# Kernel optimization log

Measured on AMD Instinct MI355X. Metric: run time of the kernel, lower is better.

## Reference

```python
import jax, jax.numpy as jnp
import numpy as np

IN_F = 4096
OUT_F = 4096
SEQ = 4          # sequence_length: values per codeword
NCODES = 65535   # codeword 65535 is reserved as escape in the original


def setup_inputs() -> dict:
    key = jax.random.key(0)
    k1, k2, k3, k4 = jax.random.split(key, 4)
    x = jax.random.normal(k1, (4, 2048, IN_F), dtype=jnp.float32)
    # compression table: codeword -> length-SEQ sequence of uint8 values
    table = jax.random.randint(k2, (NCODES, SEQ), 0, 256, dtype=jnp.int32)
    # compressed weight stream: OUT_F*IN_F/SEQ codeword indices
    codes = jax.random.randint(k3, (OUT_F * IN_F // SEQ,), 0, NCODES, dtype=jnp.int32)
    bias = jax.random.normal(k4, (OUT_F,), dtype=jnp.float32)
    return {"x": x, "table": table, "codes": codes, "bias": bias}


def reference(x, table, codes, bias):
    # decompress_weights: gather each codeword's sequence, flatten, view as (out, in)
    w = table[codes].reshape(OUT_F, IN_F).astype(jnp.float32)  # [O, I]
    # F.linear(x, w, bias) = x @ w.T + bias
    return jnp.einsum('bsi,oi->bso', x, w) + bias
```

## Files before the change

### kernel.cpp

```cpp
#include <hip/hip_runtime.h>

#define IN_F 4096
#define OUT_F 4096
#define M_DIM 8192
#define NT 32

typedef __attribute__((ext_vector_type(4))) int i32x4;
typedef unsigned short u16;

typedef const __attribute__((address_space(1))) void* gas_t;
typedef __attribute__((address_space(3))) void* las_t;

__device__ __forceinline__ void async16(const void* g, void* s) {
  __builtin_amdgcn_global_load_lds((gas_t)g, (las_t)s, 16, 0, 0);
}

__global__ void k_decompress8(const int* __restrict__ codes,
                              const int* __restrict__ table,
                              int* __restrict__ Wq) {
  int i = blockIdx.x * 256 + threadIdx.x;
  int4 c = *(const int4*)(codes + (size_t)i * 4);
  int4 t0 = *(const int4*)(table + (size_t)c.x * 4);
  int4 t1 = *(const int4*)(table + (size_t)c.y * 4);
  int4 t2 = *(const int4*)(table + (size_t)c.z * 4);
  int4 t3 = *(const int4*)(table + (size_t)c.w * 4);
  int4 o;
  o.x = (t0.x | (t0.y << 8) | (t0.z << 16) | (t0.w << 24)) ^ 0x80808080;
  o.y = (t1.x | (t1.y << 8) | (t1.z << 16) | (t1.w << 24)) ^ 0x80808080;
  o.z = (t2.x | (t2.y << 8) | (t2.z << 16) | (t2.w << 24)) ^ 0x80808080;
  o.w = (t3.x | (t3.y << 8) | (t3.z << 16) | (t3.w << 24)) ^ 0x80808080;
  *(int4*)(Wq + (size_t)i * 4) = o;
}

__global__ __launch_bounds__(256) void k_quantize(const float* __restrict__ x,
                                                  int* __restrict__ xq,
                                                  float* __restrict__ s,
                                                  float* __restrict__ rs2) {
  __shared__ float2 sred[4];
  const int row = blockIdx.x, t = threadIdx.x;
  const float4* xr = (const float4*)(x + (size_t)row * IN_F);
  float4 v[4];
  float amax = 0.f, sum = 0.f;
#pragma unroll
  for (int i = 0; i < 4; ++i) {
    v[i] = xr[t + i * 256];
    amax = fmaxf(amax, fmaxf(fmaxf(fabsf(v[i].x), fabsf(v[i].y)),
                             fmaxf(fabsf(v[i].z), fabsf(v[i].w))));
    sum += v[i].x + v[i].y + v[i].z + v[i].w;
  }
#pragma unroll
  for (int m = 1; m < 64; m <<= 1) {
    amax = fmaxf(amax, __shfl_xor(amax, m));
    sum += __shfl_xor(sum, m);
  }
  if ((t & 63) == 0) sred[t >> 6] = make_float2(amax, sum);
  __syncthreads();
  float2 r0 = sred[0], r1 = sred[1], r2 = sred[2], r3 = sred[3];
  amax = fmaxf(fmaxf(r0.x, r1.x), fmaxf(r2.x, r3.x));
  sum = r0.y + r1.y + r2.y + r3.y;
  const float inv = amax > 0.f ? 127.f / amax : 0.f;
  if (t == 0) { s[row] = amax / 127.f; rs2[row] = 128.f * sum; }
  int* xo = xq + (size_t)row * (IN_F / 4);
#pragma unroll
  for (int i = 0; i < 4; ++i) {
    int q0 = min(127, max(-127, __float2int_rn(v[i].x * inv)));
    int q1 = min(127, max(-127, __float2int_rn(v[i].y * inv)));
    int q2 = min(127, max(-127, __float2int_rn(v[i].z * inv)));
    int q3 = min(127, max(-127, __float2int_rn(v[i].w * inv)));
    xo[t + i * 256] = (q0 & 255) | ((q1 & 255) << 8) | ((q2 & 255) << 16) |
                      ((q3 & 255) << 24);
  }
}

#define BAR()    asm volatile("s_barrier" ::: "memory")
#define WAITV6() asm volatile("s_waitcnt vmcnt(6)" ::: "memory")
#define WAITV4() asm volatile("s_waitcnt vmcnt(4)" ::: "memory")
#define WAITV0() asm volatile("s_waitcnt vmcnt(0)" ::: "memory")
#define SBAR()   __builtin_amdgcn_sched_barrier(0)
#define MFMAI(va, vb, vc) __builtin_amdgcn_mfma_i32_16x16x64_i8((va), (vb), (vc), 0, 0, 0)

__global__ __launch_bounds__(512, 2) void k_gemm_i8(
    const char* __restrict__ Xq, const char* __restrict__ Wq,
    const float* __restrict__ s, const float* __restrict__ rs2,
    const float* __restrict__ bias, float* __restrict__ out) {
  extern __shared__ char sm[];
  const int tid = threadIdx.x;
  const int w = tid >> 6, ln = tid & 63;
  const int wr = w >> 2, wc = w & 3;

  const int orig = blockIdx.x;
  const int wg = (orig & 7) * 64 + (orig >> 3);
  const int bm0 = (wg >> 4) * 256;
  const int bn0 = (wg & 15) * 256;

  const int srow = ln >> 3;
  const int sg = ((ln & 7) ^ srow) * 16;
  const char* pA = Xq + (size_t)(bm0 + w * 16 + srow) * IN_F + sg;
  const char* pB = Wq + (size_t)(bn0 + w * 16 + srow) * IN_F + sg;
  const int wso = w * 2048;

  const int l15 = ln & 15;
  int ccp[2];
#pragma unroll
  for (int ks = 0; ks < 2; ++ks)
    ccp[ks] = ((ks * 4 + (ln >> 4)) ^ (ln & 7)) * 16;
  const int arow = (wr * 64 + l15) * 128;
  const int brow = 65536 + (wc * 32 + l15) * 128;

#define STA(t, h, db)                                                          \
  do {                                                                         \
    async16(pA + (size_t)(t)*128 + (size_t)(h)*128 * IN_F,                     \
            sm + (db)*32768 + (h)*16384 + wso);                                \
    async16(pA + (size_t)(t)*128 + (size_t)(h)*128 * IN_F + 8 * IN_F,          \
            sm + (db)*32768 + (h)*16384 + wso + 1024);                         \
  } while (0)
#define STB(t, h, db)                                                          \
  do {                                                                         \
    async16(pB + (size_t)(t)*128 + (size_t)(h)*128 * IN_F,                     \
            sm + 65536 + (db)*32768 + (h)*16384 + wso);                        \
    async16(pB + (size_t)(t)*128 + (size_t)(h)*128 * IN_F + 8 * IN_F,          \
            sm + 65536 + (db)*32768 + (h)*16384 + wso + 1024);                 \
  } while (0)
#define RD_A0(base)                                                            \
  do {                                                                         \
    _Pragma("unroll") for (int i = 0; i < 4; ++i)                              \
        _Pragma("unroll") for (int ks = 0; ks < 2; ++ks) a0[i][ks] =           \
        *(const i32x4*)(sm + (base) + arow + i * 2048 + ccp[ks]);              \
  } while (0)
#define RD_A1(base)                                                            \
  do {                                                                         \
    _Pragma("unroll") for (int i = 0; i < 4; ++i)                              \
        _Pragma("unroll") for (int ks = 0; ks < 2; ++ks) a1[i][ks] =           \
        *(const i32x4*)(sm + (base) + arow + i * 2048 + ccp[ks]);              \
  } while (0)
#define RD_B0(base)                                                            \
  do {                                                                         \
    _Pragma("unroll") for (int bn = 0; bn < 2; ++bn)                           \
        _Pragma("unroll") for (int ks = 0; ks < 2; ++ks) b0[bn][ks] =          \
        *(const i32x4*)(sm + (base) + brow + bn * 2048 + ccp[ks]);             \
  } while (0)
#define RD_B1(base)                                                            \
  do {                                                                         \
    _Pragma("unroll") for (int bn = 0; bn < 2; ++bn)                           \
        _Pragma("unroll") for (int ks = 0; ks < 2; ++ks) b1[bn][ks] =          \
        *(const i32x4*)(sm + (base) + brow + bn * 2048 + ccp[ks]);             \
  } while (0)

  STA(0, 0, 0); STB(0, 0, 0); STB(0, 1, 0); STA(0, 1, 0);
  STA(1, 0, 1); STB(1, 0, 1); STB(1, 1, 1);
  i32x4 acc[8][4] = {};
  i32x4 a0[4][2], a1[4][2], b0[2][2], b1[2][2];
  WAITV4();
  BAR();
  RD_A0(0);
  RD_B0(0);

  for (int t = 0; t < NT; ++t) {
    const int d = t & 1, dn = d ^ 1;
    const int d32 = d * 32768, dn32 = dn * 32768;
    RD_B1(d32 + 16384);
    if (t + 1 < NT) STA(t + 1, 1, dn);
    SBAR();
    __builtin_amdgcn_s_setprio(1);
#pragma unroll
    for (int i = 0; i < 4; ++i)
#pragma unroll
      for (int bn = 0; bn < 2; ++bn) {
        acc[i][bn] = MFMAI(a0[i][0], b0[bn][0], acc[i][bn]);
        acc[i][bn] = MFMAI(a0[i][1], b0[bn][1], acc[i][bn]);
      }
    __builtin_amdgcn_s_setprio(0);
    BAR();
    RD_A1(d32 + 16384);
    if (t + 2 < NT) STA(t + 2, 0, d);
    SBAR();
    __builtin_amdgcn_s_setprio(1);
#pragma unroll
    for (int i = 0; i < 4; ++i)
#pragma unroll
      for (int bn = 0; bn < 2; ++bn) {
        acc[i][2 + bn] = MFMAI(a0[i][0], b1[bn][0], acc[i][2 + bn]);
        acc[i][2 + bn] = MFMAI(a0[i][1], b1[bn][1], acc[i][2 + bn]);
      }
    __builtin_amdgcn_s_setprio(0);
    if (t + 1 < NT) RD_A0(dn32);
    if (t + 2 < NT) STB(t + 2, 0, d);
    SBAR();
    __builtin_amdgcn_s_setprio(1);
#pragma unroll
    for (int i = 0; i < 4; ++i)
#pragma unroll
      for (int bn = 0; bn < 2; ++bn) {
        acc[4 + i][2 + bn] = MFMAI(a1[i][0], b1[bn][0], acc[4 + i][2 + bn]);
        acc[4 + i][2 + bn] = MFMAI(a1[i][1], b1[bn][1], acc[4 + i][2 + bn]);
      }
    __builtin_amdgcn_s_setprio(0);
    if (t < NT - 2) { WAITV6(); } else { WAITV0(); }
    BAR();
    if (t + 2 < NT) STB(t + 2, 1, d);
    SBAR();
    __builtin_amdgcn_s_setprio(1);
#pragma unroll
    for (int i = 0; i < 4; ++i)
#pragma unroll
      for (int bn = 0; bn < 2; ++bn) {
        acc[4 + i][bn] = MFMAI(a1[i][0], b0[bn][0], acc[4 + i][bn]);
        acc[4 + i][bn] = MFMAI(a1[i][1], b0[bn][1], acc[4 + i][bn]);
      }
    __builtin_amdgcn_s_setprio(0);
    if (t + 1 < NT) RD_B0(dn32);
    if (t < NT - 2) { WAITV4(); } else { WAITV0(); }
    BAR();
  }

  const int r4 = (ln >> 4) * 4;
#pragma unroll
  for (int im = 0; im < 8; ++im) {
    const int mq = im >> 2, i = im & 3;
    const int rowb = bm0 + mq * 128 + wr * 64 + i * 16 + r4;
    float sv[4], rv[4];
#pragma unroll
    for (int r = 0; r < 4; ++r) { sv[r] = s[rowb + r]; rv[r] = rs2[rowb + r]; }
#pragma unroll
    for (int in = 0; in < 4; ++in) {
      const int nq = in >> 1, bn = in & 1;
      const int col = bn0 + nq * 128 + wc * 32 + bn * 16 + l15;
      const float bv = bias[col];
#pragma unroll
      for (int r = 0; r < 4; ++r)
        out[(size_t)(rowb + r) * OUT_F + col] =
            fmaf(sv[r], (float)acc[im][in][r], rv[r] + bv);
    }
  }
#undef STA
#undef STB
#undef RD_A0
#undef RD_A1
#undef RD_B0
#undef RD_B1
}

__global__ void k_naive(const float* __restrict__ x, const int* __restrict__ table,
                        const int* __restrict__ codes, const float* __restrict__ bias,
                        float* __restrict__ out) {
  __shared__ float sx[IN_F];
  const int m = blockIdx.y;
  const int n = blockIdx.x * 256 + threadIdx.x;
  for (int k = threadIdx.x; k < IN_F; k += 256) sx[k] = x[(size_t)m * IN_F + k];
  __syncthreads();
  float sacc = 0.f;
  const int* cr = codes + (size_t)n * (IN_F / 4);
  for (int k4 = 0; k4 < IN_F / 4; ++k4) {
    int code = cr[k4];
    int4 tt = *(const int4*)(table + (size_t)code * 4);
    const float* xp = sx + k4 * 4;
    sacc += xp[0] * tt.x + xp[1] * tt.y + xp[2] * tt.z + xp[3] * tt.w;
  }
  out[(size_t)m * OUT_F + n] = sacc + bias[n];
}

extern "C" void kernel_launch(void* const* d_in, const int* in_sizes, int n_in,
                              void* d_out, int out_size, void* d_ws, size_t ws_size,
                              hipStream_t stream) {
  const float* x = (const float*)d_in[0];
  const int* table = (const int*)d_in[1];
  const int* codes = (const int*)d_in[2];
  const float* bias = (const float*)d_in[3];
  float* out = (float*)d_out;

  const size_t wqb = (size_t)OUT_F * IN_F;
  const size_t xqb = (size_t)M_DIM * IN_F;
  const size_t sb = (size_t)M_DIM * 4;
  if (ws_size >= wqb + xqb + 2 * sb) {
    char* Wq = (char*)d_ws;
    char* Xq = (char*)d_ws + wqb;
    float* sS = (float*)((char*)d_ws + wqb + xqb);
    float* sR = sS + M_DIM;
    k_decompress8<<<(OUT_F * IN_F / 16) / 256, 256, 0, stream>>>(codes, table,
                                                                 (int*)Wq);
    k_quantize<<<M_DIM, 256, 0, stream>>>(x, (int*)Xq, sS, sR);
    (void)hipFuncSetAttribute((const void*)k_gemm_i8,
                              hipFuncAttributeMaxDynamicSharedMemorySize, 131072);
    k_gemm_i8<<<dim3((M_DIM / 256) * (OUT_F / 256)), dim3(512), 131072, stream>>>(
        Xq, Wq, sS, sR, bias, out);
  } else {
    dim3 grid(OUT_F / 256, M_DIM);
    k_naive<<<grid, 256, 0, stream>>>(x, table, codes, bias, out);
  }
}
```

Baseline: 183.6 us.

## Fuse decompress and quantize launches; drop one GEMM barrier per k-step

Merges the weight decompression and activation quantization kernels into one launch, with the grid split by block index, to save a kernel launch and the gap between the two. In the int8 GEMM main loop it removes one workgroup barrier per iteration and moves the first half of the B-tile store after the later barrier, adding an explicit LDS-count wait. Fewer barriers shorten the synchronization overhead of the software pipeline, at the risk of LDS read/write hazards if the reordered stores overlap buffers still being read.

```diff
diff --git a/kernel.cpp b/kernel.cpp
--- a/kernel.cpp
+++ b/kernel.cpp
@@ -6,7 +6,6 @@
 #define NT 32
 
 typedef __attribute__((ext_vector_type(4))) int i32x4;
-typedef unsigned short u16;
 
 typedef const __attribute__((address_space(1))) void* gas_t;
 typedef __attribute__((address_space(3))) void* las_t;
@@ -15,29 +14,28 @@
   __builtin_amdgcn_global_load_lds((gas_t)g, (las_t)s, 16, 0, 0);
 }
 
-__global__ void k_decompress8(const int* __restrict__ codes,
-                              const int* __restrict__ table,
-                              int* __restrict__ Wq) {
-  int i = blockIdx.x * 256 + threadIdx.x;
-  int4 c = *(const int4*)(codes + (size_t)i * 4);
-  int4 t0 = *(const int4*)(table + (size_t)c.x * 4);
-  int4 t1 = *(const int4*)(table + (size_t)c.y * 4);
-  int4 t2 = *(const int4*)(table + (size_t)c.z * 4);
-  int4 t3 = *(const int4*)(table + (size_t)c.w * 4);
-  int4 o;
-  o.x = (t0.x | (t0.y << 8) | (t0.z << 16) | (t0.w << 24)) ^ 0x80808080;
-  o.y = (t1.x | (t1.y << 8) | (t1.z << 16) | (t1.w << 24)) ^ 0x80808080;
-  o.z = (t2.x | (t2.y << 8) | (t2.z << 16) | (t2.w << 24)) ^ 0x80808080;
-  o.w = (t3.x | (t3.y << 8) | (t3.z << 16) | (t3.w << 24)) ^ 0x80808080;
-  *(int4*)(Wq + (size_t)i * 4) = o;
-}
-
-__global__ __launch_bounds__(256) void k_quantize(const float* __restrict__ x,
-                                                  int* __restrict__ xq,
-                                                  float* __restrict__ s,
-                                                  float* __restrict__ rs2) {
+__global__ __launch_bounds__(256) void k_prep(
+    const float* __restrict__ x, const int* __restrict__ codes,
+    const int* __restrict__ table, int* __restrict__ xq,
+    float* __restrict__ s, float* __restrict__ rs2, int* __restrict__ Wq) {
+  const int bid = blockIdx.x, t = threadIdx.x;
+  if (bid >= M_DIM) {
+    int i = (bid - M_DIM) * 256 + t;
+    int4 c = *(const int4*)(codes + (size_t)i * 4);
+    int4 t0 = *(const int4*)(table + (size_t)c.x * 4);
+    int4 t1 = *(const int4*)(table + (size_t)c.y * 4);
+    int4 t2 = *(const int4*)(table + (size_t)c.z * 4);
+    int4 t3 = *(const int4*)(table + (size_t)c.w * 4);
+    int4 o;
+    o.x = (t0.x | (t0.y << 8) | (t0.z << 16) | (t0.w << 24)) ^ 0x80808080;
+    o.y = (t1.x | (t1.y << 8) | (t1.z << 16) | (t1.w << 24)) ^ 0x80808080;
+    o.z = (t2.x | (t2.y << 8) | (t2.z << 16) | (t2.w << 24)) ^ 0x80808080;
+    o.w = (t3.x | (t3.y << 8) | (t3.z << 16) | (t3.w << 24)) ^ 0x80808080;
+    *(int4*)(Wq + (size_t)i * 4) = o;
+    return;
+  }
   __shared__ float2 sred[4];
-  const int row = blockIdx.x, t = threadIdx.x;
+  const int row = bid;
   const float4* xr = (const float4*)(x + (size_t)row * IN_F);
   float4 v[4];
   float amax = 0.f, sum = 0.f;
@@ -76,6 +74,7 @@
 #define WAITV6() asm volatile("s_waitcnt vmcnt(6)" ::: "memory")
 #define WAITV4() asm volatile("s_waitcnt vmcnt(4)" ::: "memory")
 #define WAITV0() asm volatile("s_waitcnt vmcnt(0)" ::: "memory")
+#define WAITL0() asm volatile("s_waitcnt lgkmcnt(0)" ::: "memory")
 #define SBAR()   __builtin_amdgcn_sched_barrier(0)
 #define MFMAI(va, vb, vc) __builtin_amdgcn_mfma_i32_16x16x64_i8((va), (vb), (vc), 0, 0, 0)
 
@@ -170,7 +169,6 @@
         acc[i][bn] = MFMAI(a0[i][1], b0[bn][1], acc[i][bn]);
       }
     __builtin_amdgcn_s_setprio(0);
-    BAR();
     RD_A1(d32 + 16384);
     if (t + 2 < NT) STA(t + 2, 0, d);
     SBAR();
@@ -184,7 +182,6 @@
       }
     __builtin_amdgcn_s_setprio(0);
     if (t + 1 < NT) RD_A0(dn32);
-    if (t + 2 < NT) STB(t + 2, 0, d);
     SBAR();
     __builtin_amdgcn_s_setprio(1);
 #pragma unroll
@@ -195,9 +192,11 @@
         acc[4 + i][2 + bn] = MFMAI(a1[i][1], b1[bn][1], acc[4 + i][2 + bn]);
       }
     __builtin_amdgcn_s_setprio(0);
+    WAITL0();
+    SBAR();
     if (t < NT - 2) { WAITV6(); } else { WAITV0(); }
     BAR();
-    if (t + 2 < NT) STB(t + 2, 1, d);
+    if (t + 2 < NT) { STB(t + 2, 0, d); STB(t + 2, 1, d); }
     SBAR();
     __builtin_amdgcn_s_setprio(1);
 #pragma unroll
@@ -276,9 +275,9 @@
     char* Xq = (char*)d_ws + wqb;
     float* sS = (float*)((char*)d_ws + wqb + xqb);
     float* sR = sS + M_DIM;
-    k_decompress8<<<(OUT_F * IN_F / 16) / 256, 256, 0, stream>>>(codes, table,
-                                                                 (int*)Wq);
-    k_quantize<<<M_DIM, 256, 0, stream>>>(x, (int*)Xq, sS, sR);
+    const int prep_blocks = M_DIM + (OUT_F * IN_F / 16) / 256;
+    k_prep<<<prep_blocks, 256, 0, stream>>>(x, codes, table, (int*)Xq, sS, sR,
+                                            (int*)Wq);
     (void)hipFuncSetAttribute((const void*)k_gemm_i8,
                               hipFuncAttributeMaxDynamicSharedMemorySize, 131072);
     k_gemm_i8<<<dim3((M_DIM / 256) * (OUT_F / 256)), dim3(512), 131072, stream>>>(
```

New measurement: 180.8 us. Within noise of the previous version (-1.5%).
